# Performance work log

Hardware: AMD Instinct MI355X
Metric: run time of the kernel (lower is better)

The kernel has to match this reference:

```python
import jax, jax.numpy as jnp
import numpy as np

D_MODEL = 256
B = 4
Q_PER_IMAGE = 256
FEATS_PER_IMAGE = 65536
HW = 512


def setup_inputs() -> dict:
    key = jax.random.key(0)
    ks = jax.random.split(key, 12)
    queries = jax.random.normal(ks[0], (B * Q_PER_IMAGE, D_MODEL), dtype=jnp.float32)
    feature_values = jax.random.normal(ks[1], (B * FEATS_PER_IMAGE, D_MODEL), dtype=jnp.float32)
    # sparse COO indices of the full-scale feature map: (batch, h, w), batch-sorted
    batch_col = jnp.repeat(jnp.arange(B, dtype=jnp.int64), FEATS_PER_IMAGE)
    hw = jax.random.randint(ks[2], (B * FEATS_PER_IMAGE, 2), 0, HW).astype(jnp.int64)
    feature_indices = jnp.concatenate([batch_col[:, None], hw], axis=-1)
    query_batch_offsets = (jnp.arange(B, dtype=jnp.int64) * Q_PER_IMAGE)
    # MLP params: torch nn.Linear convention y = x @ W.T + b, W: [out, in]
    scale = 1.0 / np.sqrt(D_MODEL)
    params = {}
    for i in range(4):
        params[f"W{i+1}"] = jax.random.uniform(ks[3 + 2 * i], (D_MODEL, D_MODEL), jnp.float32, -scale, scale)
        params[f"b{i+1}"] = jax.random.uniform(ks[4 + 2 * i], (D_MODEL,), jnp.float32, -scale, scale)
    return {
        "queries": queries,
        "feature_values": feature_values,
        "feature_indices": feature_indices,
        "query_batch_offsets": query_batch_offsets,
        **params,
    }


def reference(queries, feature_values, feature_indices, query_batch_offsets,
              W1, b1, W2, b2, W3, b3, W4, b4):
    x = queries
    for W, b in ((W1, b1), (W2, b2), (W3, b3)):
        x = jax.nn.relu(x @ W.T + b)
    x = x @ W4.T + b4  # [B*Q, d]

    nb = query_batch_offsets.shape[0]
    d = x.shape[-1]
    q = x.reshape(nb, -1, d)                    # [B, Q, d] per-image query splits
    feats = feature_values.reshape(nb, -1, d)   # [B, Nf, d] per-image feature splits
    # per-image torch.mm(im_feats, im_queries.T), batched
    logits = jnp.einsum("bnd,bqd->bnq", feats, q)  # values of the output sparse COO tensor
    # Output sparse indices are (feature_indices[i], q) for each local query q;
    # the values (in index order) are exactly `logits`.
    return logits
```

## Files before the change

### kernel.cpp

```cpp
#include <hip/hip_runtime.h>
#include <hip/hip_bf16.h>

#define D_MODEL 256
#define N_ROWS  262144
#define N_Q     1024

typedef __attribute__((ext_vector_type(8))) short short8;
typedef __attribute__((ext_vector_type(16))) float floatx16;

static __device__ __forceinline__ short f2bf(float x) {
    union { __hip_bfloat16 h; short s; } u;
    u.h = __float2bfloat16(x);
    return u.s;
}

__global__ __launch_bounds__(256) void mlp_kernel(
    const float* __restrict__ q,
    const float* __restrict__ W1, const float* __restrict__ b1,
    const float* __restrict__ W2, const float* __restrict__ b2,
    const float* __restrict__ W3, const float* __restrict__ b3,
    const float* __restrict__ W4, const float* __restrict__ b4,
    __hip_bfloat16* __restrict__ xout)
{
    __shared__ float cur[4][D_MODEL];
    const int j = threadIdx.x;
    const int row0 = blockIdx.x * 4;

    #pragma unroll
    for (int i = 0; i < 4; i++)
        cur[i][j] = q[(long)(row0 + i) * D_MODEL + j];
    __syncthreads();

    const float* Ws[4] = { W1, W2, W3, W4 };
    const float* bs[4] = { b1, b2, b3, b4 };

    for (int l = 0; l < 4; l++) {
        const float4* wrow = (const float4*)(Ws[l] + (long)j * D_MODEL);
        float acc0 = bs[l][j];
        float acc1 = acc0, acc2 = acc0, acc3 = acc0;
        #pragma unroll 8
        for (int k = 0; k < D_MODEL / 4; k++) {
            float4 w  = wrow[k];
            float4 c0 = ((const float4*)cur[0])[k];
            float4 c1 = ((const float4*)cur[1])[k];
            float4 c2 = ((const float4*)cur[2])[k];
            float4 c3 = ((const float4*)cur[3])[k];
            acc0 += w.x*c0.x + w.y*c0.y + w.z*c0.z + w.w*c0.w;
            acc1 += w.x*c1.x + w.y*c1.y + w.z*c1.z + w.w*c1.w;
            acc2 += w.x*c2.x + w.y*c2.y + w.z*c2.z + w.w*c2.w;
            acc3 += w.x*c3.x + w.y*c3.y + w.z*c3.z + w.w*c3.w;
        }
        __syncthreads();
        if (l < 3) {
            cur[0][j] = fmaxf(acc0, 0.f);
            cur[1][j] = fmaxf(acc1, 0.f);
            cur[2][j] = fmaxf(acc2, 0.f);
            cur[3][j] = fmaxf(acc3, 0.f);
            __syncthreads();
        } else {
            xout[(long)(row0 + 0) * D_MODEL + j] = __float2bfloat16(acc0);
            xout[(long)(row0 + 1) * D_MODEL + j] = __float2bfloat16(acc1);
            xout[(long)(row0 + 2) * D_MODEL + j] = __float2bfloat16(acc2);
            xout[(long)(row0 + 3) * D_MODEL + j] = __float2bfloat16(acc3);
        }
    }
}

#define APAD 264

__global__ __launch_bounds__(256) void logits_kernel(
    const float* __restrict__ F,
    const __hip_bfloat16* __restrict__ X,
    float* __restrict__ out)
{
    __shared__ __hip_bfloat16 As[64 * APAD];

    const int t    = threadIdx.x;
    const int wave = t >> 6;
    const int lane = t & 63;
    const int m    = lane & 31;
    const int kg   = lane >> 5;

    const long row0  = (long)blockIdx.x * 64;
    const int  batch = (int)(row0 >> 16);

    const float* Fbase = F + row0 * D_MODEL;
    #pragma unroll
    for (int i = 0; i < 16; i++) {
        const int flat = i * 256 + t;
        const int row  = flat >> 6;
        const int c4   = (flat & 63) << 2;
        float4 v = *(const float4*)(Fbase + (size_t)flat * 4);
        union { ushort4 u; short s[4]; } w;
        w.s[0] = f2bf(v.x); w.s[1] = f2bf(v.y);
        w.s[2] = f2bf(v.z); w.s[3] = f2bf(v.w);
        *(ushort4*)(&As[row * APAD + c4]) = w.u;
    }
    __syncthreads();

    const __hip_bfloat16* a0 = &As[m * APAD + kg * 8];
    const __hip_bfloat16* a1 = a0 + 32 * APAD;
    const __hip_bfloat16* bb = X + ((long)(batch << 8) + (wave << 6) + m) * D_MODEL + kg * 8;
    const __hip_bfloat16* b0 = bb;
    const __hip_bfloat16* b1 = bb + 32 * D_MODEL;

    floatx16 acc00 = {0.f}, acc01 = {0.f}, acc10 = {0.f}, acc11 = {0.f};

    #pragma unroll 4
    for (int ks = 0; ks < 16; ks++) {
        const int k0 = ks * 16;

        short8 af0 = *(const short8*)(a0 + k0);
        short8 af1 = *(const short8*)(a1 + k0);
        short8 bf0 = *(const short8*)(b0 + k0);
        short8 bf1 = *(const short8*)(b1 + k0);

        acc00 = __builtin_amdgcn_mfma_f32_32x32x16_bf16(af0, bf0, acc00, 0, 0, 0);
        acc01 = __builtin_amdgcn_mfma_f32_32x32x16_bf16(af0, bf1, acc01, 0, 0, 0);
        acc10 = __builtin_amdgcn_mfma_f32_32x32x16_bf16(af1, bf0, acc10, 0, 0, 0);
        acc11 = __builtin_amdgcn_mfma_f32_32x32x16_bf16(af1, bf1, acc11, 0, 0, 0);
    }

    const int colbase = (wave << 6) + m;
    #pragma unroll
    for (int rt = 0; rt < 2; rt++) {
        const floatx16 accr0 = (rt == 0) ? acc00 : acc10;
        const floatx16 accr1 = (rt == 0) ? acc01 : acc11;
        const long rbase = row0 + rt * 32 + 4 * kg;
        #pragma unroll
        for (int reg = 0; reg < 16; reg++) {
            const int r = (reg & 3) + 8 * (reg >> 2);
            out[(rbase + r) * D_MODEL + colbase]      = accr0[reg];
            out[(rbase + r) * D_MODEL + colbase + 32] = accr1[reg];
        }
    }
}

extern "C" void kernel_launch(void* const* d_in, const int* in_sizes, int n_in,
                              void* d_out, int out_size, void* d_ws, size_t ws_size,
                              hipStream_t stream) {
    const float* queries = (const float*)d_in[0];
    const float* feats   = (const float*)d_in[1];
    const float* W1 = (const float*)d_in[4];
    const float* b1 = (const float*)d_in[5];
    const float* W2 = (const float*)d_in[6];
    const float* b2 = (const float*)d_in[7];
    const float* W3 = (const float*)d_in[8];
    const float* b3 = (const float*)d_in[9];
    const float* W4 = (const float*)d_in[10];
    const float* b4 = (const float*)d_in[11];

    __hip_bfloat16* x_bf16 = (__hip_bfloat16*)d_ws;

    mlp_kernel<<<N_Q / 4, 256, 0, stream>>>(queries, W1, b1, W2, b2, W3, b3, W4, b4, x_bf16);
    logits_kernel<<<N_ROWS / 64, 256, 0, stream>>>(feats, x_bf16, (float*)d_out);
}
```

Measured before the change: 551.9 us.

## Load feature rows directly into MFMA fragments, drop LDS staging, nontemporal stores

The logits kernel stops staging the fp32 feature tile through shared memory with a barrier. Each wave now reads its own 32 rows straight from global memory, converts them to bf16 in registers and runs them against four 32-column query tiles, using a 2x2 wave layout instead of four column waves. Output stores become nontemporal and launch bounds request 4 blocks per CU. This removes LDS traffic and the sync, but each feature row is now read only by the two waves that cover it, with strided per-lane global loads that may coalesce less well.

```diff
diff --git a/kernel.cpp b/kernel.cpp
--- a/kernel.cpp
+++ b/kernel.cpp
@@ -66,73 +66,61 @@
     }
 }
 
-#define APAD 264
-
-__global__ __launch_bounds__(256) void logits_kernel(
+__global__ __launch_bounds__(256, 4) void logits_kernel(
     const float* __restrict__ F,
     const __hip_bfloat16* __restrict__ X,
     float* __restrict__ out)
 {
-    __shared__ __hip_bfloat16 As[64 * APAD];
-
     const int t    = threadIdx.x;
     const int wave = t >> 6;
     const int lane = t & 63;
     const int m    = lane & 31;
     const int kg   = lane >> 5;
+    const int wr   = wave >> 1;
+    const int wc   = wave & 1;
 
     const long row0  = (long)blockIdx.x * 64;
     const int  batch = (int)(row0 >> 16);
 
-    const float* Fbase = F + row0 * D_MODEL;
-    #pragma unroll
-    for (int i = 0; i < 16; i++) {
-        const int flat = i * 256 + t;
-        const int row  = flat >> 6;
-        const int c4   = (flat & 63) << 2;
-        float4 v = *(const float4*)(Fbase + (size_t)flat * 4);
-        union { ushort4 u; short s[4]; } w;
-        w.s[0] = f2bf(v.x); w.s[1] = f2bf(v.y);
-        w.s[2] = f2bf(v.z); w.s[3] = f2bf(v.w);
-        *(ushort4*)(&As[row * APAD + c4]) = w.u;
-    }
-    __syncthreads();
+    const float* aptr = F + (row0 + wr * 32 + m) * D_MODEL + kg * 8;
+    const __hip_bfloat16* bptr =
+        X + ((long)(batch << 8) + (wc << 7) + m) * D_MODEL + kg * 8;
 
-    const __hip_bfloat16* a0 = &As[m * APAD + kg * 8];
-    const __hip_bfloat16* a1 = a0 + 32 * APAD;
-    const __hip_bfloat16* bb = X + ((long)(batch << 8) + (wave << 6) + m) * D_MODEL + kg * 8;
-    const __hip_bfloat16* b0 = bb;
-    const __hip_bfloat16* b1 = bb + 32 * D_MODEL;
-
-    floatx16 acc00 = {0.f}, acc01 = {0.f}, acc10 = {0.f}, acc11 = {0.f};
+    floatx16 acc0 = {0.f}, acc1 = {0.f}, acc2 = {0.f}, acc3 = {0.f};
 
     #pragma unroll 4
     for (int ks = 0; ks < 16; ks++) {
         const int k0 = ks * 16;
 
-        short8 af0 = *(const short8*)(a0 + k0);
-        short8 af1 = *(const short8*)(a1 + k0);
-        short8 bf0 = *(const short8*)(b0 + k0);
-        short8 bf1 = *(const short8*)(b1 + k0);
+        float4 alo = *(const float4*)(aptr + k0);
+        float4 ahi = *(const float4*)(aptr + k0 + 4);
+        union { short8 v; short s[8]; } af;
+        af.s[0] = f2bf(alo.x); af.s[1] = f2bf(alo.y);
+        af.s[2] = f2bf(alo.z); af.s[3] = f2bf(alo.w);
+        af.s[4] = f2bf(ahi.x); af.s[5] = f2bf(ahi.y);
+        af.s[6] = f2bf(ahi.z); af.s[7] = f2bf(ahi.w);
 
-        acc00 = __builtin_amdgcn_mfma_f32_32x32x16_bf16(af0, bf0, acc00, 0, 0, 0);
-        acc01 = __builtin_amdgcn_mfma_f32_32x32x16_bf16(af0, bf1, acc01, 0, 0, 0);
-        acc10 = __builtin_amdgcn_mfma_f32_32x32x16_bf16(af1, bf0, acc10, 0, 0, 0);
-        acc11 = __builtin_amdgcn_mfma_f32_32x32x16_bf16(af1, bf1, acc11, 0, 0, 0);
+        short8 b0 = *(const short8*)(bptr + k0);
+        short8 b1 = *(const short8*)(bptr + 32 * D_MODEL + k0);
+        short8 b2 = *(const short8*)(bptr + 64 * D_MODEL + k0);
+        short8 b3 = *(const short8*)(bptr + 96 * D_MODEL + k0);
+
+        acc0 = __builtin_amdgcn_mfma_f32_32x32x16_bf16(af.v, b0, acc0, 0, 0, 0);
+        acc1 = __builtin_amdgcn_mfma_f32_32x32x16_bf16(af.v, b1, acc1, 0, 0, 0);
+        acc2 = __builtin_amdgcn_mfma_f32_32x32x16_bf16(af.v, b2, acc2, 0, 0, 0);
+        acc3 = __builtin_amdgcn_mfma_f32_32x32x16_bf16(af.v, b3, acc3, 0, 0, 0);
     }
 
-    const int colbase = (wave << 6) + m;
+    const long rbase   = row0 + wr * 32 + 4 * kg;
+    const int  colbase = (wc << 7) + m;
     #pragma unroll
-    for (int rt = 0; rt < 2; rt++) {
-        const floatx16 accr0 = (rt == 0) ? acc00 : acc10;
-        const floatx16 accr1 = (rt == 0) ? acc01 : acc11;
-        const long rbase = row0 + rt * 32 + 4 * kg;
-        #pragma unroll
-        for (int reg = 0; reg < 16; reg++) {
-            const int r = (reg & 3) + 8 * (reg >> 2);
-            out[(rbase + r) * D_MODEL + colbase]      = accr0[reg];
-            out[(rbase + r) * D_MODEL + colbase + 32] = accr1[reg];
-        }
+    for (int reg = 0; reg < 16; reg++) {
+        const int r = (reg & 3) + 8 * (reg >> 2);
+        float* orow = out + (rbase + r) * D_MODEL + colbase;
+        __builtin_nontemporal_store(acc0[reg], orow);
+        __builtin_nontemporal_store(acc1[reg], orow + 32);
+        __builtin_nontemporal_store(acc2[reg], orow + 64);
+        __builtin_nontemporal_store(acc3[reg], orow + 96);
     }
 }
 
```

After: 630.6 us. +14.3%, slower.

## Make logits kernel persistent over tiles with register prefetch and nontemporal stores

Applied to the files above, without the earlier changes.

Each block of the logits kernel now walks 8 tiles of 32 feature rows instead of handling one 64-row tile. The next tile's fp32 features are prefetched into registers while the current tile runs its MFMAs. Blocks are remapped in a swizzled order, and output stores are marked nontemporal to avoid polluting the cache. Fewer blocks (1024) and smaller tiles cut per-block setup and let loads overlap compute. The cost is lower parallelism per block and extra syncs per tile.

```diff
diff --git a/kernel.cpp b/kernel.cpp
--- a/kernel.cpp
+++ b/kernel.cpp
@@ -67,13 +67,15 @@
 }
 
 #define APAD 264
+#define BM   32
+#define TILES_PER_BLOCK 8
 
 __global__ __launch_bounds__(256) void logits_kernel(
     const float* __restrict__ F,
     const __hip_bfloat16* __restrict__ X,
     float* __restrict__ out)
 {
-    __shared__ __hip_bfloat16 As[64 * APAD];
+    __shared__ __hip_bfloat16 As[BM * APAD];
 
     const int t    = threadIdx.x;
     const int wave = t >> 6;
@@ -81,58 +83,68 @@
     const int m    = lane & 31;
     const int kg   = lane >> 5;
 
-    const long row0  = (long)blockIdx.x * 64;
-    const int  batch = (int)(row0 >> 16);
+    int b = blockIdx.x;
+    b = (b & 7) * (1024 / 8) + (b >> 3);
 
-    const float* Fbase = F + row0 * D_MODEL;
-    #pragma unroll
-    for (int i = 0; i < 16; i++) {
-        const int flat = i * 256 + t;
-        const int row  = flat >> 6;
-        const int c4   = (flat & 63) << 2;
-        float4 v = *(const float4*)(Fbase + (size_t)flat * 4);
-        union { ushort4 u; short s[4]; } w;
-        w.s[0] = f2bf(v.x); w.s[1] = f2bf(v.y);
-        w.s[2] = f2bf(v.z); w.s[3] = f2bf(v.w);
-        *(ushort4*)(&As[row * APAD + c4]) = w.u;
-    }
-    __syncthreads();
+    const long row00 = (long)b * (BM * TILES_PER_BLOCK);
+    const int  batch = (int)(row00 >> 16);
 
-    const __hip_bfloat16* a0 = &As[m * APAD + kg * 8];
-    const __hip_bfloat16* a1 = a0 + 32 * APAD;
-    const __hip_bfloat16* bb = X + ((long)(batch << 8) + (wave << 6) + m) * D_MODEL + kg * 8;
-    const __hip_bfloat16* b0 = bb;
-    const __hip_bfloat16* b1 = bb + 32 * D_MODEL;
+    const __hip_bfloat16* bb =
+        X + ((long)(batch << 8) + (wave << 6) + m) * D_MODEL + kg * 8;
 
-    floatx16 acc00 = {0.f}, acc01 = {0.f}, acc10 = {0.f}, acc11 = {0.f};
-
-    #pragma unroll 4
-    for (int ks = 0; ks < 16; ks++) {
-        const int k0 = ks * 16;
-
-        short8 af0 = *(const short8*)(a0 + k0);
-        short8 af1 = *(const short8*)(a1 + k0);
-        short8 bf0 = *(const short8*)(b0 + k0);
-        short8 bf1 = *(const short8*)(b1 + k0);
-
-        acc00 = __builtin_amdgcn_mfma_f32_32x32x16_bf16(af0, bf0, acc00, 0, 0, 0);
-        acc01 = __builtin_amdgcn_mfma_f32_32x32x16_bf16(af0, bf1, acc01, 0, 0, 0);
-        acc10 = __builtin_amdgcn_mfma_f32_32x32x16_bf16(af1, bf0, acc10, 0, 0, 0);
-        acc11 = __builtin_amdgcn_mfma_f32_32x32x16_bf16(af1, bf1, acc11, 0, 0, 0);
+    float4 pend[8];
+    {
+        const float4* Fb = (const float4*)(F + row00 * D_MODEL);
+        #pragma unroll
+        for (int i = 0; i < 8; i++)
+            pend[i] = Fb[i * 256 + t];
     }
 
-    const int colbase = (wave << 6) + m;
-    #pragma unroll
-    for (int rt = 0; rt < 2; rt++) {
-        const floatx16 accr0 = (rt == 0) ? acc00 : acc10;
-        const floatx16 accr1 = (rt == 0) ? acc01 : acc11;
-        const long rbase = row0 + rt * 32 + 4 * kg;
+    for (int tt = 0; tt < TILES_PER_BLOCK; tt++) {
+        #pragma unroll
+        for (int i = 0; i < 8; i++) {
+            const int flat = i * 256 + t;
+            const int row  = flat >> 6;
+            const int c4   = (flat & 63) << 2;
+            union { ushort4 u; short s[4]; } w;
+            w.s[0] = f2bf(pend[i].x); w.s[1] = f2bf(pend[i].y);
+            w.s[2] = f2bf(pend[i].z); w.s[3] = f2bf(pend[i].w);
+            *(ushort4*)(&As[row * APAD + c4]) = w.u;
+        }
+        __syncthreads();
+
+        if (tt < TILES_PER_BLOCK - 1) {
+            const float4* Fb =
+                (const float4*)(F + (row00 + (long)(tt + 1) * BM) * D_MODEL);
+            #pragma unroll
+            for (int i = 0; i < 8; i++)
+                pend[i] = Fb[i * 256 + t];
+        }
+
+        const __hip_bfloat16* a0 = &As[m * APAD + kg * 8];
+        floatx16 acc0 = {0.f}, acc1 = {0.f};
+
+        #pragma unroll 4
+        for (int ks = 0; ks < 16; ks++) {
+            const int k0 = ks * 16;
+            short8 af  = *(const short8*)(a0 + k0);
+            short8 bf0 = *(const short8*)(bb + k0);
+            short8 bf1 = *(const short8*)(bb + 32 * D_MODEL + k0);
+            acc0 = __builtin_amdgcn_mfma_f32_32x32x16_bf16(af, bf0, acc0, 0, 0, 0);
+            acc1 = __builtin_amdgcn_mfma_f32_32x32x16_bf16(af, bf1, acc1, 0, 0, 0);
+        }
+
+        const long rbase   = row00 + (long)tt * BM + 4 * kg;
+        const int  colbase = (wave << 6) + m;
         #pragma unroll
         for (int reg = 0; reg < 16; reg++) {
             const int r = (reg & 3) + 8 * (reg >> 2);
-            out[(rbase + r) * D_MODEL + colbase]      = accr0[reg];
-            out[(rbase + r) * D_MODEL + colbase + 32] = accr1[reg];
+            float* orow = out + (rbase + r) * D_MODEL + colbase;
+            __builtin_nontemporal_store(acc0[reg], orow);
+            __builtin_nontemporal_store(acc1[reg], orow + 32);
         }
+
+        __syncthreads();
     }
 }
 
@@ -153,5 +165,6 @@
     __hip_bfloat16* x_bf16 = (__hip_bfloat16*)d_ws;
 
     mlp_kernel<<<N_Q / 4, 256, 0, stream>>>(queries, W1, b1, W2, b2, W3, b3, W4, b4, x_bf16);
-    logits_kernel<<<N_ROWS / 64, 256, 0, stream>>>(feats, x_bf16, (float*)d_out);
+    logits_kernel<<<N_ROWS / (BM * TILES_PER_BLOCK), 256, 0, stream>>>(
+        feats, x_bf16, (float*)d_out);
 }
```

Result: slower. 612.8 us (+11.0%).
